# Optimization experiments

Hardware: AMD Instinct MI355X
Metric: run time of the kernel (lower is better)

Reference implementation:

```python
import jax, jax.numpy as jnp
import numpy as np

SKIP = 2 ** -0.5
EPS = 1e-6
DIM = 1024
N_LAYERS = 8
N_HEADS = 16
MAX_SEQ = 1024
B = 4
L = 1024


def get_rot_emb(dim, max_seq_len):
    pos = jnp.arange(max_seq_len, dtype=jnp.float32)
    omega = 1.0 / 10000.0 ** (jnp.arange(0, dim, 2, dtype=jnp.float32) / dim)
    angles = pos[:, None] * omega[None, :]  # [S, dim/2]
    cos = jnp.repeat(jnp.cos(angles), 2, axis=-1)  # [S, dim]
    sin = jnp.repeat(jnp.sin(angles), 2, axis=-1)
    return cos, sin


def setup_inputs() -> dict:
    key = jax.random.key(0)
    ks = jax.random.split(key, 16)
    s = 0.02
    d = DIM
    nl = N_LAYERS
    cos, sin = get_rot_emb(d // N_HEADS, MAX_SEQ)
    inp = {
        'x': jax.random.normal(ks[0], (B, L, d), jnp.float32),
        'c': jax.random.normal(ks[1], (B, 1, d), jnp.float32),
        't': jax.random.normal(ks[2], (B, d), jnp.float32),
        'num_heads': N_HEADS,
        'cos': cos,
        'sin': sin,
        'qkv_w': jax.random.normal(ks[3], (nl, d, 3 * d), jnp.float32) * s,
        'qkv_b': jnp.zeros((nl, 3 * d), jnp.float32),
        'proj_w': jax.random.normal(ks[4], (nl, d, d), jnp.float32) * s,
        'proj_b': jnp.zeros((nl, d), jnp.float32),
        'mlp_w1': jax.random.normal(ks[5], (nl, d, 4 * d), jnp.float32) * s,
        'mlp_b1': jnp.zeros((nl, 4 * d), jnp.float32),
        'mlp_w2': jax.random.normal(ks[6], (nl, 4 * d, d), jnp.float32) * s,
        'mlp_b2': jnp.zeros((nl, d), jnp.float32),
        'adaln_w': jax.random.normal(ks[7], (nl, d, 6 * d), jnp.float32) * s,
        'adaln_b': jnp.zeros((nl, 6 * d), jnp.float32),
    }
    return inp


def layer_norm(x):
    mu = jnp.mean(x, axis=-1, keepdims=True)
    var = jnp.var(x, axis=-1, keepdims=True)
    return (x - mu) * jax.lax.rsqrt(var + EPS)


def rotate_half(q):
    # torch: stack([-q[..., 1::2], q[..., ::2]], -1).reshape(q.shape)
    q2 = q.reshape(q.shape[:-1] + (-1, 2))
    return jnp.stack([-q2[..., 1], q2[..., 0]], axis=-1).reshape(q.shape)


def reference(x, c, t, num_heads, cos, sin, qkv_w, qkv_b, proj_w, proj_b, mlp_w1, mlp_b1, mlp_w2, mlp_b2, adaln_w, adaln_b):
    Bx, Lx, C = x.shape
    H = int(num_heads)
    D = C // H
    scale = D ** -0.5
    cmod = (c + t[:, None]) * SKIP  # [B,1,C]
    cos_l = cos[:Lx]  # [L,D]
    sin_l = sin[:Lx]

    def block(xcur, p):
        qw, qb, pw, pb, w1, b1, w2, b2, aw, ab = p
        mod = jax.nn.silu(cmod) @ aw + ab  # [B,1,6C]
        sh1, sc1, g1, sh2, sc2, g2 = jnp.split(mod, 6, axis=-1)
        h = (layer_norm(xcur) * (1 + sc1) + sh1) * SKIP
        qkv = (h @ qw + qb).reshape(Bx, Lx, 3, H, D).transpose(2, 0, 3, 1, 4)
        q, k, v = qkv[0], qkv[1], qkv[2]  # [B,H,L,D]
        q = q * cos_l + rotate_half(q) * sin_l
        k = k * cos_l + rotate_half(k) * sin_l
        attn = jax.nn.softmax(scale * jnp.einsum('bhid,bhjd->bhij', q, k), axis=-1)
        o = jnp.einsum('bhij,bhjd->bhid', attn, v).transpose(0, 2, 1, 3).reshape(Bx, Lx, C)
        o = o @ pw + pb
        xcur = (xcur + g1 * o) * SKIP
        h2 = (layer_norm(xcur) * (1 + sc2) + sh2) * SKIP
        m = jax.nn.gelu(h2 @ w1 + b1, approximate=True) @ w2 + b2
        return (xcur + g2 * m) * SKIP, None

    params = (qkv_w, qkv_b, proj_w, proj_b, mlp_w1, mlp_b1, mlp_w2, mlp_b2, adaln_w, adaln_b)
    out, _ = jax.lax.scan(block, x, params)
    return out
```

## Files before the change

kernel.cpp:

```cpp
#include <hip/hip_runtime.h>

#define SKIPF 0.70710678118654752440f

typedef unsigned short u16;
typedef unsigned int u32;
typedef __attribute__((ext_vector_type(4))) short bf16x4;
typedef __attribute__((ext_vector_type(8))) short bf16x8;
typedef __attribute__((ext_vector_type(4))) float f32x4;

#define MFMA32(A, B, C) __builtin_amdgcn_mfma_f32_16x16x32_bf16(A, B, C, 0, 0, 0)
#define MFMA16(A, B, C) __builtin_amdgcn_mfma_f32_16x16x16bf16_1k(A, B, C, 0, 0, 0)

__device__ __forceinline__ float bf2f(u16 v) {
  u32 u = ((u32)v) << 16; float f; __builtin_memcpy(&f, &u, 4); return f;
}
__device__ __forceinline__ u16 f2bf(float f) {
  u32 u; __builtin_memcpy(&u, &f, 4);
  u = (u + 0x7fffu + ((u >> 16) & 1u)) >> 16;
  return (u16)u;
}
__device__ __forceinline__ void gload16(const void* g, void* s) {
  __builtin_amdgcn_global_load_lds((const __attribute__((address_space(1))) void*)g,
                                   (__attribute__((address_space(3))) void*)s, 16, 0, 0);
}


__global__ void copy_f32_kernel(const float4* __restrict__ src, float4* __restrict__ dst, int n) {
  int i = blockIdx.x * blockDim.x + threadIdx.x;
  if (i < n) dst[i] = src[i];
}

__global__ void silu_prep_kernel(const float* __restrict__ c, const float* __restrict__ t,
                                 float* __restrict__ silu_c) {
  int i = blockIdx.x * 256 + threadIdx.x;
  float x = (c[i] + t[i]) * SKIPF;
  silu_c[i] = x / (1.f + __expf(-x));
}

__global__ void adaln_part_kernel(const float* __restrict__ silu_c, const float* __restrict__ aw,
                                  float* __restrict__ part) {
  __shared__ float sc[4][64];
  int n = blockIdx.x * 256 + threadIdx.x;
  int ks = blockIdx.y;
  int k0 = ks * 64;
  int b = threadIdx.x >> 6, kk = threadIdx.x & 63;
  sc[b][kk] = silu_c[b * 1024 + k0 + kk];
  __syncthreads();
  float a0 = 0.f, a1 = 0.f, a2 = 0.f, a3 = 0.f;
  for (int k = 0; k < 64; ++k) {
    float w = aw[(size_t)(k0 + k) * 6144 + n];
    a0 += sc[0][k] * w; a1 += sc[1][k] * w; a2 += sc[2][k] * w; a3 += sc[3][k] * w;
  }
  part[(size_t)(ks * 4 + 0) * 6144 + n] = a0;
  part[(size_t)(ks * 4 + 1) * 6144 + n] = a1;
  part[(size_t)(ks * 4 + 2) * 6144 + n] = a2;
  part[(size_t)(ks * 4 + 3) * 6144 + n] = a3;
}

__global__ void adaln_reduce_kernel(const float* __restrict__ part, const float* __restrict__ ab,
                                    float* __restrict__ mod) {
  int i = blockIdx.x * 256 + threadIdx.x;
  int b = i / 6144, n = i - b * 6144;
  float a = ab[n];
  for (int ks = 0; ks < 16; ++ks) a += part[(size_t)(ks * 4 + b) * 6144 + n];
  mod[(size_t)b * 6144 + n] = a;
}

__global__ void wtrans_kernel(const float* __restrict__ W, u16* __restrict__ WT, int K, int N) {
  __shared__ float tile[32][33];
  int n0 = blockIdx.x * 32, k0 = blockIdx.y * 32;
  int tx = threadIdx.x, ty = threadIdx.y;
#pragma unroll
  for (int i = 0; i < 4; ++i)
    tile[ty * 4 + i][tx] = W[(size_t)(k0 + ty * 4 + i) * N + n0 + tx];
  __syncthreads();
#pragma unroll
  for (int i = 0; i < 4; ++i)
    WT[(size_t)(n0 + ty * 4 + i) * K + k0 + tx] = f2bf(tile[tx][ty * 4 + i]);
}

__global__ __launch_bounds__(256) void ln_mod_kernel(const float* __restrict__ x,
                                                     const float* __restrict__ mod,
                                                     u16* __restrict__ h, int sh_off, int sc_off) {
  int row = blockIdx.x;
  int b = row >> 10;
  const float4* xr = (const float4*)(x + (size_t)row * 1024);
  float4 v = xr[threadIdx.x];
  float s = v.x + v.y + v.z + v.w;
  float ss = v.x * v.x + v.y * v.y + v.z * v.z + v.w * v.w;
#pragma unroll
  for (int o = 32; o; o >>= 1) { s += __shfl_xor(s, o); ss += __shfl_xor(ss, o); }
  __shared__ float red[8];
  int wave = threadIdx.x >> 6;
  if ((threadIdx.x & 63) == 0) { red[wave * 2] = s; red[wave * 2 + 1] = ss; }
  __syncthreads();
  s = red[0] + red[2] + red[4] + red[6];
  ss = red[1] + red[3] + red[5] + red[7];
  float mu = s * (1.f / 1024.f);
  float var = ss * (1.f / 1024.f) - mu * mu;
  float rs = rsqrtf(var + 1e-6f);
  int n = threadIdx.x * 4;
  const float* mb = mod + (size_t)b * 6144;
  float4 sc = *(const float4*)(mb + sc_off + n);
  float4 sh = *(const float4*)(mb + sh_off + n);
  ushort4 o4;
  o4.x = f2bf(((v.x - mu) * rs * (1.f + sc.x) + sh.x) * SKIPF);
  o4.y = f2bf(((v.y - mu) * rs * (1.f + sc.y) + sh.y) * SKIPF);
  o4.z = f2bf(((v.z - mu) * rs * (1.f + sc.z) + sh.z) * SKIPF);
  o4.w = f2bf(((v.w - mu) * rs * (1.f + sc.w) + sh.w) * SKIPF);
  *(ushort4*)(h + (size_t)row * 1024 + n) = o4;
}

template <int EPI>
__global__ __launch_bounds__(512, 1) void gemm256r_kernel(
    const u16* __restrict__ A, const u16* __restrict__ BT, const float* __restrict__ bias,
    u16* __restrict__ Cb, int NBX, int N, int K) {
  __shared__ u16 lds[4][16384];
  const int tid = threadIdx.x;
  const int lane = tid & 63, wave = tid >> 6;
  const int lq = lane & 15, lk = lane >> 4;
  const int wr = wave >> 2, wc = wave & 3;

  int per = gridDim.x >> 3;
  int swz = (blockIdx.x & 7) * per + (blockIdx.x >> 3);
  int bx = swz % NBX, by = swz / NBX;
  const int m0 = by * 256, n0 = bx * 256;

  f32x4 acc[8][4];
#pragma unroll
  for (int i = 0; i < 8; ++i)
#pragma unroll
    for (int j = 0; j < 4; ++j) acc[i][j] = (f32x4){0.f, 0.f, 0.f, 0.f};

  auto STAGE = [&](int slot, int t) {
    int kt = t * 32;
    char* Ab = (char*)lds[slot];
    char* Bb = (char*)(lds[slot] + 8192);
#pragma unroll
    for (int q = 0; q < 2; ++q) {
      int u = tid + q * 512;
      int r = u >> 3, cpos = u & 7;
      int g = cpos ^ (r & 7);
      gload16(A + (size_t)(m0 + 2 * r + (g >> 2)) * K + kt + (g & 3) * 8, Ab + u * 16);
    }
#pragma unroll
    for (int q = 0; q < 2; ++q) {
      int u = tid + q * 512;
      int r = u >> 3, cpos = u & 7;
      int g = cpos ^ (r & 7);
      gload16(BT + (size_t)(n0 + 2 * r + (g >> 2)) * K + kt + (g & 3) * 8, Bb + u * 16);
    }
  };

  const int NT = K >> 5;
  STAGE(0, 0); STAGE(1, 1); STAGE(2, 2);
  int slot = 0;
  for (int t = 0; t < NT; ++t) {
    int rem = NT - 1 - t;
    if (rem >= 2) asm volatile("s_waitcnt vmcnt(8)" ::: "memory");
    else if (rem == 1) asm volatile("s_waitcnt vmcnt(4)" ::: "memory");
    else asm volatile("s_waitcnt vmcnt(0)" ::: "memory");
    __builtin_amdgcn_s_barrier();
    __builtin_amdgcn_sched_barrier(0);
    if (t + 3 < NT) { int ns = slot + 3; if (ns >= 4) ns -= 4; STAGE(ns, t + 3); }
    const char* Ab = (const char*)lds[slot];
    const char* Bb = (const char*)(lds[slot] + 8192);
    bf16x8 bfr[4];
#pragma unroll
    for (int ni = 0; ni < 4; ++ni) {
      int nrow = wc * 64 + ni * 16 + lq;
      int r = nrow >> 1, g = (nrow & 1) * 4 + lk;
      bfr[ni] = *(const bf16x8*)(Bb + r * 128 + ((g ^ (r & 7)) << 4));
    }
#pragma unroll
    for (int ph = 0; ph < 4; ++ph) {
      bf16x8 af0, af1;
      {
        int mrow = wr * 128 + (ph * 2) * 16 + lq;
        int r = mrow >> 1, g = (mrow & 1) * 4 + lk;
        af0 = *(const bf16x8*)(Ab + r * 128 + ((g ^ (r & 7)) << 4));
        mrow += 16;
        r = mrow >> 1; g = (mrow & 1) * 4 + lk;
        af1 = *(const bf16x8*)(Ab + r * 128 + ((g ^ (r & 7)) << 4));
      }
      __builtin_amdgcn_s_setprio(1);
#pragma unroll
      for (int j = 0; j < 4; ++j) acc[ph * 2][j] = MFMA32(af0, bfr[j], acc[ph * 2][j]);
#pragma unroll
      for (int j = 0; j < 4; ++j) acc[ph * 2 + 1][j] = MFMA32(af1, bfr[j], acc[ph * 2 + 1][j]);
      __builtin_amdgcn_s_setprio(0);
    }
    ++slot; if (slot >= 4) slot = 0;
  }

#pragma unroll
  for (int i = 0; i < 8; ++i) {
    int rbase = m0 + wr * 128 + i * 16 + lk * 4;
#pragma unroll
    for (int j = 0; j < 4; ++j) {
      int cg = n0 + wc * 64 + j * 16 + lq;
      float bv = bias[cg];
#pragma unroll
      for (int r = 0; r < 4; ++r) {
        int row = rbase + r;
        float val = acc[i][j][r] + bv;
        if (EPI == 0) {
          Cb[(size_t)row * N + cg] = f2bf(val);
        } else {
          float tt = 0.7978845608028654f * (val + 0.044715f * val * val * val);
          float e = __expf(2.f * tt);
          float th = 1.f - 2.f / (e + 1.f);
          Cb[(size_t)row * N + cg] = f2bf(0.5f * val * (1.f + th));
        }
      }
    }
  }
}

__global__ __launch_bounds__(256) void gemm_res_kernel(
    const u16* __restrict__ A, const u16* __restrict__ BT, const float* __restrict__ bias,
    float* __restrict__ xio, const float* __restrict__ mod, int g_off, int K) {
  __shared__ u16 As[2][64 * 32];
  __shared__ u16 Bs[2][128 * 32];
  const int tid = threadIdx.x;
  const int lane = tid & 63, wave = tid >> 6;
  const int lq = lane & 15, lk = lane >> 4;
  const int wr = wave >> 1, wc = wave & 1;
  const int m0 = blockIdx.y * 64, n0 = blockIdx.x * 128;

  const int srow = tid >> 2;
  const int skc = (tid & 3) * 8;
  const u16* Ag = A + (size_t)(m0 + (srow & 63)) * K + skc;
  const u16* Bg = BT + (size_t)(n0 + srow) * K + skc;

  f32x4 acc[2][4];
#pragma unroll
  for (int i = 0; i < 2; ++i)
#pragma unroll
    for (int j = 0; j < 4; ++j) acc[i][j] = (f32x4){0.f, 0.f, 0.f, 0.f};

  auto STAGE = [&](int buf, int kt) {
    char* ab = (char*)As[buf];
    char* bb = (char*)Bs[buf];
    if (tid < 256) {
      if ((tid >> 2) < 64) gload16(Ag + kt, ab + tid * 16);
    }
    gload16(Bg + kt, bb + tid * 16);
    gload16(Bg + (size_t)64 * K + kt, bb + 4096 + tid * 16);
  };

  STAGE(0, 0);
  __syncthreads();
  int cur = 0;
  for (int kt = 0; kt < K; kt += 32) {
    if (kt + 32 < K) STAGE(cur ^ 1, kt + 32);
    const bf16x8* Av = (const bf16x8*)As[cur];
    const bf16x8* Bv = (const bf16x8*)Bs[cur];
    bf16x8 af[2], bfr[4];
#pragma unroll
    for (int i = 0; i < 2; ++i) af[i] = Av[(wr * 32 + i * 16 + lq) * 4 + lk];
#pragma unroll
    for (int j = 0; j < 4; ++j) bfr[j] = Bv[(wc * 64 + j * 16 + lq) * 4 + lk];
#pragma unroll
    for (int i = 0; i < 2; ++i)
#pragma unroll
      for (int j = 0; j < 4; ++j) acc[i][j] = MFMA32(af[i], bfr[j], acc[i][j]);
    __syncthreads();
    cur ^= 1;
  }

#pragma unroll
  for (int i = 0; i < 2; ++i) {
    int rbase = m0 + wr * 32 + i * 16 + lk * 4;
#pragma unroll
    for (int j = 0; j < 4; ++j) {
      int cg = n0 + wc * 64 + j * 16 + lq;
      float bv = bias[cg];
#pragma unroll
      for (int r = 0; r < 4; ++r) {
        int row = rbase + r;
        float val = acc[i][j][r] + bv;
        int b = row >> 10;
        float g = mod[(size_t)b * 6144 + g_off + cg];
        float xv = xio[(size_t)row * 1024 + cg];
        xio[(size_t)row * 1024 + cg] = (xv + g * val) * SKIPF;
      }
    }
  }
}

__global__ __launch_bounds__(256) void ropev_kernel(
    const u16* __restrict__ qkv, const float* __restrict__ cosb, const float* __restrict__ sinb,
    u16* __restrict__ qo, u16* __restrict__ ko, u16* __restrict__ vt) {
  __shared__ u16 tile[64][72];
  int bh = blockIdx.y, l0 = blockIdx.x * 64;
  int b = bh >> 4, h = bh & 15;
  int r = threadIdx.x >> 2, c = (threadIdx.x & 3) * 16;
  int l = l0 + r;
  const u16* src = qkv + (size_t)(b * 1024 + l) * 3072 + h * 64 + c;
  *(uint4*)&tile[r][c] = *(const uint4*)(src + 2048);
  *(uint4*)&tile[r][c + 8] = *(const uint4*)(src + 2048 + 8);
  size_t dst_off = ((size_t)bh * 1024 + l) * 64 + c;
#pragma unroll
  for (int qk = 0; qk < 2; ++qk) {
    const u16* s2 = src + qk * 1024;
    u32 w0[4], w1[4];
#pragma unroll
    for (int p = 0; p < 8; ++p) {
      u32 pr = *(const u32*)(s2 + p * 2);
      int d0 = c + p * 2;
      float cc = cosb[l * 64 + d0], sn = sinb[l * 64 + d0];
      float e0 = bf2f((u16)(pr & 0xffff)), e1 = bf2f((u16)(pr >> 16));
      u32 ow = (u32)f2bf(e0 * cc - e1 * sn) | ((u32)f2bf(e1 * cc + e0 * sn) << 16);
      if (p < 4) w0[p] = ow; else w1[p - 4] = ow;
    }
    u16* dst = (qk ? ko : qo) + dst_off;
    uint4 v0; v0.x = w0[0]; v0.y = w0[1]; v0.z = w0[2]; v0.w = w0[3];
    uint4 v1; v1.x = w1[0]; v1.y = w1[1]; v1.z = w1[2]; v1.w = w1[3];
    *(uint4*)dst = v0;
    *(uint4*)(dst + 8) = v1;
  }
  __syncthreads();
  int d = threadIdx.x >> 2, lc = threadIdx.x & 3;
  u16 tmp[16];
#pragma unroll
  for (int j = 0; j < 16; ++j) tmp[j] = tile[lc * 16 + j][d];
  u16* dstv = vt + ((size_t)bh * 64 + d) * 1024 + l0 + lc * 16;
  *(uint4*)dstv = *(uint4*)tmp;
  *(uint4*)(dstv + 8) = *(uint4*)(tmp + 8);
}

__global__ __launch_bounds__(256) void attn_kernel(const u16* __restrict__ qb,
                                                   const u16* __restrict__ kb,
                                                   const u16* __restrict__ vt,
                                                   u16* __restrict__ ob) {
  __shared__ u16 ktile[2][4096];
  __shared__ u16 vtile[2][4096];
  int nid = (blockIdx.x & 7) * 64 + (blockIdx.x >> 3);
  int qt = nid & 7, bh = nid >> 3;
  int tid = threadIdx.x;
  int lane = tid & 63, wave = tid >> 6;
  int lq = lane & 15, lk = lane >> 4;
  const u16* Q = qb + (size_t)bh * 65536;
  const u16* Kp = kb + (size_t)bh * 65536;
  const u16* VT = vt + (size_t)bh * 65536;
  int qbase = qt * 128 + wave * 32;

  bf16x8 qf[2][2];
#pragma unroll
  for (int g = 0; g < 2; ++g) {
    qf[g][0] = *(const bf16x8*)(Q + (size_t)(qbase + g * 16 + lq) * 64 + lk * 8);
    qf[g][1] = *(const bf16x8*)(Q + (size_t)(qbase + g * 16 + lq) * 64 + 32 + lk * 8);
  }

  auto stage_one = [&](int buf, int kvb, int u) {
    int r = u >> 3;
    int cc = ((u & 7) ^ (r & 7)) * 8;
    gload16(Kp + (size_t)(kvb + r) * 64 + cc, (char*)ktile[buf] + u * 16);
    gload16(VT + (size_t)r * 1024 + kvb + cc, (char*)vtile[buf] + u * 16);
  };

  float mrun[2] = {-1e30f, -1e30f}, lsum[2] = {0.f, 0.f};
  f32x4 oacc[2][4];
#pragma unroll
  for (int g = 0; g < 2; ++g)
#pragma unroll
    for (int f = 0; f < 4; ++f) oacc[g][f] = (f32x4){0.f, 0.f, 0.f, 0.f};
  const f32x4 z4 = (f32x4){0.f, 0.f, 0.f, 0.f};

  stage_one(0, 0, tid);
  stage_one(0, 0, tid + 256);
  __syncthreads();
  int cur = 0;
  for (int t = 0; t < 16; ++t) {
    if (t < 15) {
      stage_one(cur ^ 1, (t + 1) * 64, tid);
      stage_one(cur ^ 1, (t + 1) * 64, tid + 256);
    }
    const char* kb_ = (const char*)ktile[cur];
    const char* vb_ = (const char*)vtile[cur];
    f32x4 st[2][4];
#pragma unroll
    for (int s = 0; s < 4; ++s) {
      int r = s * 16 + lq;
      int sw = (r & 7) << 4;
      bf16x8 kf0 = *(const bf16x8*)(kb_ + r * 128 + ((lk * 16) ^ sw));
      bf16x8 kf1 = *(const bf16x8*)(kb_ + r * 128 + ((64 + lk * 16) ^ sw));
      st[0][s] = MFMA32(kf0, qf[0][0], z4);
      st[0][s] = MFMA32(kf1, qf[0][1], st[0][s]);
      st[1][s] = MFMA32(kf0, qf[1][0], z4);
      st[1][s] = MFMA32(kf1, qf[1][1], st[1][s]);
    }
    bf16x4 pf[2][4];
#pragma unroll
    for (int g = 0; g < 2; ++g) {
      float pm = -1e30f;
#pragma unroll
      for (int s = 0; s < 4; ++s)
#pragma unroll
        for (int r = 0; r < 4; ++r) {
          st[g][s][r] *= 0.125f;
          pm = fmaxf(pm, st[g][s][r]);
        }
      pm = fmaxf(pm, __shfl_xor(pm, 16));
      pm = fmaxf(pm, __shfl_xor(pm, 32));
      if (!__all(pm - mrun[g] <= 8.f)) {
        float mnew = fmaxf(mrun[g], pm);
        float corr = __expf(mrun[g] - mnew);
        float c0 = __shfl(corr, lk * 4 + 0), c1 = __shfl(corr, lk * 4 + 1);
        float c2 = __shfl(corr, lk * 4 + 2), c3 = __shfl(corr, lk * 4 + 3);
#pragma unroll
        for (int f = 0; f < 4; ++f) {
          oacc[g][f][0] *= c0; oacc[g][f][1] *= c1;
          oacc[g][f][2] *= c2; oacc[g][f][3] *= c3;
        }
        lsum[g] *= corr;
        mrun[g] = mnew;
      }
      float ps = 0.f;
#pragma unroll
      for (int s = 0; s < 4; ++s) {
        float p0 = __expf(st[g][s][0] - mrun[g]);
        float p1 = __expf(st[g][s][1] - mrun[g]);
        float p2 = __expf(st[g][s][2] - mrun[g]);
        float p3 = __expf(st[g][s][3] - mrun[g]);
        ps += p0 + p1 + p2 + p3;
        pf[g][s][0] = (short)f2bf(p0); pf[g][s][1] = (short)f2bf(p1);
        pf[g][s][2] = (short)f2bf(p2); pf[g][s][3] = (short)f2bf(p3);
      }
      ps += __shfl_xor(ps, 16);
      ps += __shfl_xor(ps, 32);
      lsum[g] += ps;
    }
#pragma unroll
    for (int f = 0; f < 4; ++f) {
      int r = lq + f * 16;
      int sw = (r & 7) << 4;
#pragma unroll
      for (int s = 0; s < 4; ++s) {
        bf16x4 vf = *(const bf16x4*)(vb_ + r * 128 + ((s * 32 + lk * 8) ^ sw));
        oacc[0][f] = MFMA16(pf[0][s], vf, oacc[0][f]);
        oacc[1][f] = MFMA16(pf[1][s], vf, oacc[1][f]);
      }
    }
    __syncthreads();
    cur ^= 1;
  }

  int b = bh >> 4, hh = bh & 15;
#pragma unroll
  for (int g = 0; g < 2; ++g) {
    float inv = 1.f / lsum[g];
    float i0 = __shfl(inv, lk * 4 + 0), i1 = __shfl(inv, lk * 4 + 1);
    float i2 = __shfl(inv, lk * 4 + 2), i3 = __shfl(inv, lk * 4 + 3);
#pragma unroll
    for (int f = 0; f < 4; ++f) {
#pragma unroll
      for (int j = 0; j < 4; ++j) {
        int qrow = qbase + g * 16 + lk * 4 + j;
        float sc = (j == 0) ? i0 : (j == 1) ? i1 : (j == 2) ? i2 : i3;
        ob[((size_t)(b * 1024 + qrow)) * 1024 + hh * 64 + lq + f * 16] = f2bf(oacc[g][f][j] * sc);
      }
    }
  }
}


extern "C" void kernel_launch(void* const* d_in, const int* in_sizes, int n_in,
                              void* d_out, int out_size, void* d_ws, size_t ws_size,
                              hipStream_t stream) {
  const float* x = (const float*)d_in[0];
  const float* c = (const float*)d_in[1];
  const float* t = (const float*)d_in[2];
  const float* cosb = (const float*)d_in[4];
  const float* sinb = (const float*)d_in[5];
  const float* qkv_w = (const float*)d_in[6];
  const float* qkv_b = (const float*)d_in[7];
  const float* proj_w = (const float*)d_in[8];
  const float* proj_b = (const float*)d_in[9];
  const float* w1 = (const float*)d_in[10];
  const float* b1 = (const float*)d_in[11];
  const float* w2 = (const float*)d_in[12];
  const float* b2 = (const float*)d_in[13];
  const float* aw = (const float*)d_in[14];
  const float* ab = (const float*)d_in[15];

  constexpr size_t OFF_X = 0;
  constexpr size_t OFF_H = OFF_X + 16777216;
  constexpr size_t OFF_BIG = OFF_H + 8388608;
  constexpr size_t OFF_Q = OFF_BIG + 33554432;
  constexpr size_t OFF_K = OFF_Q + 8388608;
  constexpr size_t OFF_V = OFF_K + 8388608;
  constexpr size_t OFF_AO = OFF_V + 8388608;
  constexpr size_t OFF_WQ = OFF_AO + 8388608;
  constexpr size_t OFF_WP = OFF_WQ + 6291456;
  constexpr size_t OFF_W1 = OFF_WP + 2097152;
  constexpr size_t OFF_W2 = OFF_W1 + 8388608;
  constexpr size_t OFF_SC = OFF_W2 + 8388608;
  constexpr size_t OFF_MOD = OFF_SC + 16384;
  constexpr size_t OFF_PART = OFF_MOD + 98304;

  char* ws = (char*)d_ws;
  float* x_cur = (float*)(ws + OFF_X);
  u16* h = (u16*)(ws + OFF_H);
  u16* big = (u16*)(ws + OFF_BIG);
  u16* qv = (u16*)(ws + OFF_Q);
  u16* kv = (u16*)(ws + OFF_K);
  u16* vt = (u16*)(ws + OFF_V);
  u16* ao = (u16*)(ws + OFF_AO);
  u16* wTq = (u16*)(ws + OFF_WQ);
  u16* wTp = (u16*)(ws + OFF_WP);
  u16* wT1 = (u16*)(ws + OFF_W1);
  u16* wT2 = (u16*)(ws + OFF_W2);
  float* silu_c = (float*)(ws + OFF_SC);
  float* mod = (float*)(ws + OFF_MOD);
  float* part = (float*)(ws + OFF_PART);

  copy_f32_kernel<<<4096, 256, 0, stream>>>((const float4*)x, (float4*)x_cur, 1048576);
  silu_prep_kernel<<<16, 256, 0, stream>>>(c, t, silu_c);

  for (int L = 0; L < 8; ++L) {
    const float* awL = aw + (size_t)L * 1024 * 6144;
    const float* abL = ab + (size_t)L * 6144;
    const float* qwL = qkv_w + (size_t)L * 1024 * 3072;
    const float* qbL = qkv_b + (size_t)L * 3072;
    const float* pwL = proj_w + (size_t)L * 1024 * 1024;
    const float* pbL = proj_b + (size_t)L * 1024;
    const float* w1L = w1 + (size_t)L * 1024 * 4096;
    const float* b1L = b1 + (size_t)L * 4096;
    const float* w2L = w2 + (size_t)L * 4096 * 1024;
    const float* b2L = b2 + (size_t)L * 1024;

    adaln_part_kernel<<<dim3(24, 16), 256, 0, stream>>>(silu_c, awL, part);
    adaln_reduce_kernel<<<96, 256, 0, stream>>>(part, abL, mod);

    wtrans_kernel<<<dim3(96, 32), dim3(32, 8), 0, stream>>>(qwL, wTq, 1024, 3072);
    wtrans_kernel<<<dim3(32, 32), dim3(32, 8), 0, stream>>>(pwL, wTp, 1024, 1024);
    wtrans_kernel<<<dim3(128, 32), dim3(32, 8), 0, stream>>>(w1L, wT1, 1024, 4096);
    wtrans_kernel<<<dim3(32, 128), dim3(32, 8), 0, stream>>>(w2L, wT2, 4096, 1024);

    ln_mod_kernel<<<4096, 256, 0, stream>>>(x_cur, mod, h, 0, 1024);
    gemm256r_kernel<0><<<192, 512, 0, stream>>>(h, wTq, qbL, big, 12, 3072, 1024);
    ropev_kernel<<<dim3(16, 64), 256, 0, stream>>>(big, cosb, sinb, qv, kv, vt);
    attn_kernel<<<512, 256, 0, stream>>>(qv, kv, vt, ao);
    gemm_res_kernel<<<dim3(8, 64), 256, 0, stream>>>(ao, wTp, pbL, x_cur, mod, 2048, 1024);
    ln_mod_kernel<<<4096, 256, 0, stream>>>(x_cur, mod, h, 3072, 4096);
    gemm256r_kernel<1><<<256, 512, 0, stream>>>(h, wT1, b1L, big, 16, 4096, 1024);
    gemm_res_kernel<<<dim3(8, 64), 256, 0, stream>>>(big, wT2, b2L, x_cur, mod, 5120, 4096);
  }

  copy_f32_kernel<<<4096, 256, 0, stream>>>((const float4*)x_cur, (float4*)d_out, 1048576);
}
```

Measured before the change: 2.190 ms.

## Triple-buffer GEMM and attention loads, drop residual copy kernels

Moves the residual GEMM and attention K/V staging from double to triple buffering, with explicit vmcnt waits and a single barrier per iteration, so loads run two tiles ahead. Raises MFMA wave priority with setprio. Removes the initial and final copy kernels by reading x directly in layer 0 and writing d_out in layer 7. This uses more LDS per block, which may lower occupancy, and the hand-written waitcnt counts must match the number of issued loads.

Measured after the change: 2.208 ms. About the same (+0.8%).

```diff
diff --git a/kernel.cpp b/kernel.cpp
--- a/kernel.cpp
+++ b/kernel.cpp
@@ -24,11 +24,6 @@
                                    (__attribute__((address_space(3))) void*)s, 16, 0, 0);
 }
 
-
-__global__ void copy_f32_kernel(const float4* __restrict__ src, float4* __restrict__ dst, int n) {
-  int i = blockIdx.x * blockDim.x + threadIdx.x;
-  if (i < n) dst[i] = src[i];
-}
 
 __global__ void silu_prep_kernel(const float* __restrict__ c, const float* __restrict__ t,
                                  float* __restrict__ silu_c) {
@@ -79,12 +74,12 @@
     WT[(size_t)(n0 + ty * 4 + i) * K + k0 + tx] = f2bf(tile[tx][ty * 4 + i]);
 }
 
-__global__ __launch_bounds__(256) void ln_mod_kernel(const float* __restrict__ x,
+__global__ __launch_bounds__(256) void ln_mod_kernel(const float* __restrict__ xin,
                                                      const float* __restrict__ mod,
                                                      u16* __restrict__ h, int sh_off, int sc_off) {
   int row = blockIdx.x;
   int b = row >> 10;
-  const float4* xr = (const float4*)(x + (size_t)row * 1024);
+  const float4* xr = (const float4*)(xin + (size_t)row * 1024);
   float4 v = xr[threadIdx.x];
   float s = v.x + v.y + v.z + v.w;
   float ss = v.x * v.x + v.y * v.y + v.z * v.z + v.w * v.w;
@@ -219,9 +214,10 @@
 
 __global__ __launch_bounds__(256) void gemm_res_kernel(
     const u16* __restrict__ A, const u16* __restrict__ BT, const float* __restrict__ bias,
-    float* __restrict__ xio, const float* __restrict__ mod, int g_off, int K) {
-  __shared__ u16 As[2][64 * 32];
-  __shared__ u16 Bs[2][128 * 32];
+    const float* __restrict__ xin, float* __restrict__ xout, const float* __restrict__ mod,
+    int g_off, int K) {
+  __shared__ u16 As[3][64 * 32];
+  __shared__ u16 Bs[3][128 * 32];
   const int tid = threadIdx.x;
   const int lane = tid & 63, wave = tid >> 6;
   const int lq = lane & 15, lk = lane >> 4;
@@ -230,7 +226,7 @@
 
   const int srow = tid >> 2;
   const int skc = (tid & 3) * 8;
-  const u16* Ag = A + (size_t)(m0 + (srow & 63)) * K + skc;
+  const u16* Ag = A + (size_t)(m0 + srow) * K + skc;
   const u16* Bg = BT + (size_t)(n0 + srow) * K + skc;
 
   f32x4 acc[2][4];
@@ -239,34 +235,36 @@
 #pragma unroll
     for (int j = 0; j < 4; ++j) acc[i][j] = (f32x4){0.f, 0.f, 0.f, 0.f};
 
-  auto STAGE = [&](int buf, int kt) {
-    char* ab = (char*)As[buf];
-    char* bb = (char*)Bs[buf];
-    if (tid < 256) {
-      if ((tid >> 2) < 64) gload16(Ag + kt, ab + tid * 16);
-    }
-    gload16(Bg + kt, bb + tid * 16);
-    gload16(Bg + (size_t)64 * K + kt, bb + 4096 + tid * 16);
+  auto STAGE = [&](int slot, int t) {
+    int kt = t * 32;
+    gload16(Ag + kt, (char*)As[slot] + tid * 16);
+    gload16(Bg + kt, (char*)Bs[slot] + tid * 16);
+    gload16(Bg + (size_t)64 * K + kt, (char*)Bs[slot] + 4096 + tid * 16);
   };
 
-  STAGE(0, 0);
-  __syncthreads();
-  int cur = 0;
-  for (int kt = 0; kt < K; kt += 32) {
-    if (kt + 32 < K) STAGE(cur ^ 1, kt + 32);
-    const bf16x8* Av = (const bf16x8*)As[cur];
-    const bf16x8* Bv = (const bf16x8*)Bs[cur];
+  const int NT = K >> 5;
+  STAGE(0, 0); STAGE(1, 1);
+  int slot = 0;
+  for (int t = 0; t < NT; ++t) {
+    if (t + 1 < NT) asm volatile("s_waitcnt vmcnt(3)" ::: "memory");
+    else asm volatile("s_waitcnt vmcnt(0)" ::: "memory");
+    __builtin_amdgcn_s_barrier();
+    __builtin_amdgcn_sched_barrier(0);
+    if (t + 2 < NT) { int ns = slot + 2; if (ns >= 3) ns -= 3; STAGE(ns, t + 2); }
+    const bf16x8* Av = (const bf16x8*)As[slot];
+    const bf16x8* Bv = (const bf16x8*)Bs[slot];
     bf16x8 af[2], bfr[4];
 #pragma unroll
     for (int i = 0; i < 2; ++i) af[i] = Av[(wr * 32 + i * 16 + lq) * 4 + lk];
 #pragma unroll
     for (int j = 0; j < 4; ++j) bfr[j] = Bv[(wc * 64 + j * 16 + lq) * 4 + lk];
+    __builtin_amdgcn_s_setprio(1);
 #pragma unroll
     for (int i = 0; i < 2; ++i)
 #pragma unroll
       for (int j = 0; j < 4; ++j) acc[i][j] = MFMA32(af[i], bfr[j], acc[i][j]);
-    __syncthreads();
-    cur ^= 1;
+    __builtin_amdgcn_s_setprio(0);
+    ++slot; if (slot >= 3) slot = 0;
   }
 
 #pragma unroll
@@ -282,8 +280,8 @@
         float val = acc[i][j][r] + bv;
         int b = row >> 10;
         float g = mod[(size_t)b * 6144 + g_off + cg];
-        float xv = xio[(size_t)row * 1024 + cg];
-        xio[(size_t)row * 1024 + cg] = (xv + g * val) * SKIPF;
+        float xv = xin[(size_t)row * 1024 + cg];
+        xout[(size_t)row * 1024 + cg] = (xv + g * val) * SKIPF;
       }
     }
   }
@@ -334,8 +332,8 @@
                                                    const u16* __restrict__ kb,
                                                    const u16* __restrict__ vt,
                                                    u16* __restrict__ ob) {
-  __shared__ u16 ktile[2][4096];
-  __shared__ u16 vtile[2][4096];
+  __shared__ u16 ktile[3][4096];
+  __shared__ u16 vtile[3][4096];
   int nid = (blockIdx.x & 7) * 64 + (blockIdx.x >> 3);
   int qt = nid & 7, bh = nid >> 3;
   int tid = threadIdx.x;
@@ -368,18 +366,23 @@
     for (int f = 0; f < 4; ++f) oacc[g][f] = (f32x4){0.f, 0.f, 0.f, 0.f};
   const f32x4 z4 = (f32x4){0.f, 0.f, 0.f, 0.f};
 
-  stage_one(0, 0, tid);
-  stage_one(0, 0, tid + 256);
-  __syncthreads();
-  int cur = 0;
+  stage_one(0, 0, tid); stage_one(0, 0, tid + 256);
+  stage_one(1, 64, tid); stage_one(1, 64, tid + 256);
+  int slot = 0;
   for (int t = 0; t < 16; ++t) {
-    if (t < 15) {
-      stage_one(cur ^ 1, (t + 1) * 64, tid);
-      stage_one(cur ^ 1, (t + 1) * 64, tid + 256);
-    }
-    const char* kb_ = (const char*)ktile[cur];
-    const char* vb_ = (const char*)vtile[cur];
+    if (t < 15) asm volatile("s_waitcnt vmcnt(4)" ::: "memory");
+    else asm volatile("s_waitcnt vmcnt(0)" ::: "memory");
+    __builtin_amdgcn_s_barrier();
+    __builtin_amdgcn_sched_barrier(0);
+    if (t + 2 < 16) {
+      int ns = slot + 2; if (ns >= 3) ns -= 3;
+      stage_one(ns, (t + 2) * 64, tid);
+      stage_one(ns, (t + 2) * 64, tid + 256);
+    }
+    const char* kb_ = (const char*)ktile[slot];
+    const char* vb_ = (const char*)vtile[slot];
     f32x4 st[2][4];
+    __builtin_amdgcn_s_setprio(1);
 #pragma unroll
     for (int s = 0; s < 4; ++s) {
       int r = s * 16 + lq;
@@ -391,6 +394,7 @@
       st[1][s] = MFMA32(kf0, qf[1][0], z4);
       st[1][s] = MFMA32(kf1, qf[1][1], st[1][s]);
     }
+    __builtin_amdgcn_s_setprio(0);
     bf16x4 pf[2][4];
 #pragma unroll
     for (int g = 0; g < 2; ++g) {
@@ -432,6 +436,7 @@
       ps += __shfl_xor(ps, 32);
       lsum[g] += ps;
     }
+    __builtin_amdgcn_s_setprio(1);
 #pragma unroll
     for (int f = 0; f < 4; ++f) {
       int r = lq + f * 16;
@@ -443,8 +448,8 @@
         oacc[1][f] = MFMA16(pf[1][s], vf, oacc[1][f]);
       }
     }
-    __syncthreads();
-    cur ^= 1;
+    __builtin_amdgcn_s_setprio(0);
+    ++slot; if (slot >= 3) slot = 0;
   }
 
   int b = bh >> 4, hh = bh & 15;
@@ -516,7 +521,6 @@
   float* mod = (float*)(ws + OFF_MOD);
   float* part = (float*)(ws + OFF_PART);
 
-  copy_f32_kernel<<<4096, 256, 0, stream>>>((const float4*)x, (float4*)x_cur, 1048576);
   silu_prep_kernel<<<16, 256, 0, stream>>>(c, t, silu_c);
 
   for (int L = 0; L < 8; ++L) {
@@ -531,6 +535,9 @@
     const float* w2L = w2 + (size_t)L * 4096 * 1024;
     const float* b2L = b2 + (size_t)L * 1024;
 
+    const float* xin = (L == 0) ? x : x_cur;
+    float* xout2 = (L == 7) ? (float*)d_out : x_cur;
+
     adaln_part_kernel<<<dim3(24, 16), 256, 0, stream>>>(silu_c, awL, part);
     adaln_reduce_kernel<<<96, 256, 0, stream>>>(part, abL, mod);
 
@@ -539,15 +546,13 @@
     wtrans_kernel<<<dim3(128, 32), dim3(32, 8), 0, stream>>>(w1L, wT1, 1024, 4096);
     wtrans_kernel<<<dim3(32, 128), dim3(32, 8), 0, stream>>>(w2L, wT2, 4096, 1024);
 
-    ln_mod_kernel<<<4096, 256, 0, stream>>>(x_cur, mod, h, 0, 1024);
+    ln_mod_kernel<<<4096, 256, 0, stream>>>(xin, mod, h, 0, 1024);
     gemm256r_kernel<0><<<192, 512, 0, stream>>>(h, wTq, qbL, big, 12, 3072, 1024);
     ropev_kernel<<<dim3(16, 64), 256, 0, stream>>>(big, cosb, sinb, qv, kv, vt);
     attn_kernel<<<512, 256, 0, stream>>>(qv, kv, vt, ao);
-    gemm_res_kernel<<<dim3(8, 64), 256, 0, stream>>>(ao, wTp, pbL, x_cur, mod, 2048, 1024);
+    gemm_res_kernel<<<dim3(8, 64), 256, 0, stream>>>(ao, wTp, pbL, xin, x_cur, mod, 2048, 1024);
     ln_mod_kernel<<<4096, 256, 0, stream>>>(x_cur, mod, h, 3072, 4096);
     gemm256r_kernel<1><<<256, 512, 0, stream>>>(h, wT1, b1L, big, 16, 4096, 1024);
-    gemm_res_kernel<<<dim3(8, 64), 256, 0, stream>>>(big, wT2, b2L, x_cur, mod, 5120, 4096);
-  }
-
-  copy_f32_kernel<<<4096, 256, 0, stream>>>((const float4*)x_cur, (float4*)d_out, 1048576);
-}
+    gemm_res_kernel<<<dim3(8, 64), 256, 0, stream>>>(big, wT2, b2L, x_cur, xout2, mod, 5120, 4096);
+  }
+}
```
